# Optimization experiments

Hardware: AMD Instinct MI355X
Metric: run time of the kernel (lower is better)

The kernel has to match this reference:

```python
import jax, jax.numpy as jnp
import numpy as np

N_NODES = 100000
N_EDGES = 625000
D = 128       # in_features == edim
OUT = 2       # out_classes

def setup_inputs() -> dict:
    key = jax.random.key(0)
    k1, k2, k3, k4, k5, k6 = jax.random.split(key, 6)
    nfeats = jax.random.normal(k1, (N_NODES, D), dtype=jnp.float32)
    efeats = jax.random.normal(k2, (N_EDGES, D), dtype=jnp.float32)
    src = jax.random.randint(k3, (N_EDGES,), 0, N_NODES, dtype=jnp.int64)
    dst = jax.random.randint(k4, (N_EDGES,), 0, N_NODES, dtype=jnp.int64)
    # nn.Linear(2*D + D, OUT): weight [OUT, 3D], bias [OUT]
    W = jax.random.normal(k5, (OUT, 3 * D), dtype=jnp.float32) * 0.05
    b = jax.random.normal(k6, (OUT,), dtype=jnp.float32) * 0.05
    return {"nfeats": nfeats, "efeats": efeats, "src": src, "dst": dst, "W": W, "b": b}

def reference(nfeats, efeats, src, dst, W, b):
    # gather per-edge endpoint features, concat with edge feats (residual=True)
    h_src = nfeats[src]            # [E, D]
    h_dst = nfeats[dst]            # [E, D]
    h = jnp.concatenate([h_src, h_dst, efeats], axis=-1)  # [E, 3D]
    score = h @ W.T + b            # [E, OUT]
    return score
```

## Files before the change

kernel.cpp:

```cpp
#include <hip/hip_runtime.h>


static constexpr int D = 128;
static constexpr int THREADS = 256;
static constexpr int GPB = THREADS / 32;

typedef float f32x4 __attribute__((ext_vector_type(4)));

__global__ __launch_bounds__(THREADS) void node_partial_kernel(
    const float* __restrict__ nfeats,
    const float* __restrict__ W,
    float*       __restrict__ pf,
    int N)
{
    const int sl   = threadIdx.x & 31;
    const int gib  = threadIdx.x >> 5;
    const int g0   = blockIdx.x * GPB + gib;
    const int ngrp = gridDim.x * GPB;

    const float4 w0s = *reinterpret_cast<const float4*>(W +   0 + 4 * sl);
    const float4 w1s = *reinterpret_cast<const float4*>(W + 384 + 4 * sl);
    const float4 w0d = *reinterpret_cast<const float4*>(W + 128 + 4 * sl);
    const float4 w1d = *reinterpret_cast<const float4*>(W + 384 + 128 + 4 * sl);

    for (int n = g0 * 2; n + 1 < N; n += ngrp * 2) {
        float v[8];
        #pragma unroll
        for (int j = 0; j < 2; ++j) {
            const f32x4 h = __builtin_nontemporal_load(
                reinterpret_cast<const f32x4*>(nfeats + (size_t)(n + j) * D + 4 * sl));
            v[j*4+0] = h.x * w0s.x + h.y * w0s.y + h.z * w0s.z + h.w * w0s.w;
            v[j*4+1] = h.x * w1s.x + h.y * w1s.y + h.z * w1s.z + h.w * w1s.w;
            v[j*4+2] = h.x * w0d.x + h.y * w0d.y + h.z * w0d.z + h.w * w0d.w;
            v[j*4+3] = h.x * w1d.x + h.y * w1d.y + h.z * w1d.z + h.w * w1d.w;
        }
        float a4[4];
        #pragma unroll
        for (int c = 0; c < 4; ++c) {
            float send = (sl & 16) ? v[c] : v[c+4];
            float keep = (sl & 16) ? v[c+4] : v[c];
            a4[c] = keep + __shfl_xor(send, 16);
        }
        float a2[2];
        #pragma unroll
        for (int c = 0; c < 2; ++c) {
            float send = (sl & 8) ? a4[c] : a4[c+2];
            float keep = (sl & 8) ? a4[c+2] : a4[c];
            a2[c] = keep + __shfl_xor(send, 8);
        }
        float y;
        {
            float send = (sl & 4) ? a2[0] : a2[1];
            float keep = (sl & 4) ? a2[1] : a2[0];
            y = keep + __shfl_xor(send, 4);
        }
        y += __shfl_xor(y, 2);
        y += __shfl_xor(y, 1);
        if ((sl & 3) == 0) {
            pf[4 * (size_t)n + (sl >> 2)] = y;
        }
    }
}

__global__ __launch_bounds__(THREADS) void edge_kernel(
    const float*  __restrict__ efeats,
    const int*    __restrict__ src,
    const int*    __restrict__ dst,
    const float*  __restrict__ W,
    const float*  __restrict__ bias,
    const float*  __restrict__ pf,
    float*        __restrict__ out,
    int E)
{
    const int sl   = threadIdx.x & 31;
    const int gib  = threadIdx.x >> 5;
    const int g0   = blockIdx.x * GPB + gib;
    const int ngrp = gridDim.x * GPB;
    const int step = ngrp * 8;

    const float4 w0e = *reinterpret_cast<const float4*>(W + 256 + 4 * sl);
    const float4 w1e = *reinterpret_cast<const float4*>(W + 384 + 256 + 4 * sl);

    const bool wr   = (sl & 1) == 0;
    const int  myj  = sl >> 2;
    const int  myo  = (sl >> 1) & 1;
    const float myb = myo ? bias[1] : bias[0];

    int e = g0 * 8;
    if (e + 7 >= E) return;

    f32x4 he[8];
    #pragma unroll
    for (int j = 0; j < 8; ++j)
        he[j] = __builtin_nontemporal_load(
            reinterpret_cast<const f32x4*>(efeats + (size_t)(e + j) * D + 4 * sl));
    int sidx = 0, didx = 0;
    if (wr) {
        sidx = src[e + myj];
        didx = dst[e + myj];
    }

    while (e + 7 < E) {
        const int  en   = e + step;
        const bool more = (en + 7 < E);

        float ps = 0.f, pd = 0.f;
        if (wr) {
            ps = pf[(size_t)sidx * 4 + myo];
            pd = pf[(size_t)didx * 4 + 2 + myo];
        }

        float v[16];
        #pragma unroll
        for (int j = 0; j < 8; ++j) {
            v[2*j]   = he[j].x * w0e.x + he[j].y * w0e.y + he[j].z * w0e.z + he[j].w * w0e.w;
            v[2*j+1] = he[j].x * w1e.x + he[j].y * w1e.y + he[j].z * w1e.z + he[j].w * w1e.w;
        }

        if (more) {
            #pragma unroll
            for (int j = 0; j < 8; ++j)
                he[j] = __builtin_nontemporal_load(
                    reinterpret_cast<const f32x4*>(efeats + (size_t)(en + j) * D + 4 * sl));
            if (wr) {
                sidx = src[en + myj];
                didx = dst[en + myj];
            }
        }

        float a8[8];
        #pragma unroll
        for (int c = 0; c < 8; ++c) {
            float send = (sl & 16) ? v[c] : v[c+8];
            float keep = (sl & 16) ? v[c+8] : v[c];
            a8[c] = keep + __shfl_xor(send, 16);
        }
        float a4[4];
        #pragma unroll
        for (int c = 0; c < 4; ++c) {
            float send = (sl & 8) ? a8[c] : a8[c+4];
            float keep = (sl & 8) ? a8[c+4] : a8[c];
            a4[c] = keep + __shfl_xor(send, 8);
        }
        float a2[2];
        #pragma unroll
        for (int c = 0; c < 2; ++c) {
            float send = (sl & 4) ? a4[c] : a4[c+2];
            float keep = (sl & 4) ? a4[c+2] : a4[c];
            a2[c] = keep + __shfl_xor(send, 4);
        }
        float y;
        {
            float send = (sl & 2) ? a2[0] : a2[1];
            float keep = (sl & 2) ? a2[1] : a2[0];
            y = keep + __shfl_xor(send, 2);
        }
        y += __shfl_xor(y, 1);

        if (wr) {
            out[2 * (size_t)e + (sl >> 1)] = y + ps + pd + myb;
        }

        e = en;
    }
}

__global__ __launch_bounds__(THREADS) void mlp_pred_fused_kernel(
    const float* __restrict__ nfeats, const float* __restrict__ efeats,
    const int* __restrict__ src, const int* __restrict__ dst,
    const float* __restrict__ W, const float* __restrict__ bias,
    float* __restrict__ out, int E)
{
    const int sl = threadIdx.x & 31;
    const int gib = threadIdx.x >> 5;
    const int g0 = blockIdx.x * GPB + gib;
    const int ngrp = gridDim.x * GPB;

    const float4 w0s = *reinterpret_cast<const float4*>(W +   0 + 4 * sl);
    const float4 w0d = *reinterpret_cast<const float4*>(W + 128 + 4 * sl);
    const float4 w0e = *reinterpret_cast<const float4*>(W + 256 + 4 * sl);
    const float4 w1s = *reinterpret_cast<const float4*>(W + 384 +   0 + 4 * sl);
    const float4 w1d = *reinterpret_cast<const float4*>(W + 384 + 128 + 4 * sl);
    const float4 w1e = *reinterpret_cast<const float4*>(W + 384 + 256 + 4 * sl);
    const float b0 = bias[0];
    const float b1 = bias[1];

    for (int e = g0; e < E; e += ngrp) {
        const int si = src[e];
        const int di = dst[e];
        const float4 hs = *reinterpret_cast<const float4*>(nfeats + (size_t)si * D + 4 * sl);
        const float4 hd = *reinterpret_cast<const float4*>(nfeats + (size_t)di * D + 4 * sl);
        const float4 he = *reinterpret_cast<const float4*>(efeats + (size_t)e  * D + 4 * sl);

        float a0 = hs.x * w0s.x + hs.y * w0s.y + hs.z * w0s.z + hs.w * w0s.w;
        a0 += hd.x * w0d.x + hd.y * w0d.y + hd.z * w0d.z + hd.w * w0d.w;
        a0 += he.x * w0e.x + he.y * w0e.y + he.z * w0e.z + he.w * w0e.w;
        float a1 = hs.x * w1s.x + hs.y * w1s.y + hs.z * w1s.z + hs.w * w1s.w;
        a1 += hd.x * w1d.x + hd.y * w1d.y + hd.z * w1d.z + hd.w * w1d.w;
        a1 += he.x * w1e.x + he.y * w1e.y + he.z * w1e.z + he.w * w1e.w;

        #pragma unroll
        for (int off = 16; off; off >>= 1) {
            a0 += __shfl_xor(a0, off);
            a1 += __shfl_xor(a1, off);
        }
        if (sl == 0)
            *reinterpret_cast<float2*>(out + 2 * (size_t)e) = make_float2(a0 + b0, a1 + b1);
    }
}

extern "C" void kernel_launch(void* const* d_in, const int* in_sizes, int n_in,
                              void* d_out, int out_size, void* d_ws, size_t ws_size,
                              hipStream_t stream) {
    const float* nfeats = (const float*)d_in[0];
    const float* efeats = (const float*)d_in[1];
    const int*   src    = (const int*)d_in[2];
    const int*   dst    = (const int*)d_in[3];
    const float* W      = (const float*)d_in[4];
    const float* bias   = (const float*)d_in[5];
    float*       out    = (float*)d_out;

    const int E = in_sizes[2];
    const int N = in_sizes[0] / D;

    const size_t p_bytes = (size_t)N * 4 * sizeof(float);

    if (ws_size >= p_bytes && (E & 7) == 0 && (N & 1) == 0) {
        float* pf = (float*)d_ws;

        int groups1 = N / 2;
        int blocks1 = (groups1 + GPB - 1) / GPB;
        if (blocks1 > 2048) blocks1 = 2048;
        node_partial_kernel<<<blocks1, THREADS, 0, stream>>>(nfeats, W, pf, N);

        int groups2 = E / 8;
        int blocks2 = (groups2 + GPB - 1) / GPB;
        if (blocks2 > 2048) blocks2 = 2048;
        edge_kernel<<<blocks2, THREADS, 0, stream>>>(efeats, src, dst, W, bias, pf, out, E);
    } else {
        int blocks = (E + GPB - 1) / GPB;
        if (blocks > 2048) blocks = 2048;
        mlp_pred_fused_kernel<<<blocks, THREADS, 0, stream>>>(nfeats, efeats, src, dst, W, bias, out, E);
    }
}
```

Baseline: 71.74 us.

## Double-buffer edge feature loads and prefetch node rows in partial kernel

The edge kernel now keeps two register batches of edge features and indices, issuing loads two iterations ahead so more memory requests are in flight per wave. The node partial kernel gains a one-iteration software prefetch of its node rows, and output stores become nontemporal. The goal is to hide HBM latency in this bandwidth-bound streaming workload. The cost is higher register pressure from holding two 8x float4 batches, which may reduce occupancy.

After: 70.66 us. Within noise of the previous version (-1.5%).

```diff
diff --git a/kernel.cpp b/kernel.cpp
--- a/kernel.cpp
+++ b/kernel.cpp
@@ -6,6 +6,60 @@
 static constexpr int GPB = THREADS / 32;
 
 typedef float f32x4 __attribute__((ext_vector_type(4)));
+
+__device__ __forceinline__ void load_batch(f32x4 (&he)[8], const float* __restrict__ efeats,
+                                           int e, int sl) {
+    #pragma unroll
+    for (int j = 0; j < 8; ++j)
+        he[j] = __builtin_nontemporal_load(
+            reinterpret_cast<const f32x4*>(efeats + (size_t)(e + j) * D + 4 * sl));
+}
+
+__device__ __forceinline__ void fma_batch(float (&v)[16], const f32x4 (&he)[8],
+                                          const float4& w0e, const float4& w1e) {
+    #pragma unroll
+    for (int j = 0; j < 8; ++j) {
+        v[2*j]   = he[j].x * w0e.x + he[j].y * w0e.y + he[j].z * w0e.z + he[j].w * w0e.w;
+        v[2*j+1] = he[j].x * w1e.x + he[j].y * w1e.y + he[j].z * w1e.z + he[j].w * w1e.w;
+    }
+}
+
+__device__ __forceinline__ void fold_store(const float (&v)[16], int sl, bool wr,
+                                           float ps, float pd, float myb,
+                                           float* __restrict__ out, int e) {
+    float a8[8];
+    #pragma unroll
+    for (int c = 0; c < 8; ++c) {
+        float send = (sl & 16) ? v[c] : v[c+8];
+        float keep = (sl & 16) ? v[c+8] : v[c];
+        a8[c] = keep + __shfl_xor(send, 16);
+    }
+    float a4[4];
+    #pragma unroll
+    for (int c = 0; c < 4; ++c) {
+        float send = (sl & 8) ? a8[c] : a8[c+4];
+        float keep = (sl & 8) ? a8[c+4] : a8[c];
+        a4[c] = keep + __shfl_xor(send, 8);
+    }
+    float a2[2];
+    #pragma unroll
+    for (int c = 0; c < 2; ++c) {
+        float send = (sl & 4) ? a4[c] : a4[c+2];
+        float keep = (sl & 4) ? a4[c+2] : a4[c];
+        a2[c] = keep + __shfl_xor(send, 4);
+    }
+    float y;
+    {
+        float send = (sl & 2) ? a2[0] : a2[1];
+        float keep = (sl & 2) ? a2[1] : a2[0];
+        y = keep + __shfl_xor(send, 2);
+    }
+    y += __shfl_xor(y, 1);
+
+    if (wr) {
+        __builtin_nontemporal_store(y + ps + pd + myb, out + 2 * (size_t)e + (sl >> 1));
+    }
+}
 
 __global__ __launch_bounds__(THREADS) void node_partial_kernel(
     const float* __restrict__ nfeats,
@@ -17,23 +71,40 @@
     const int gib  = threadIdx.x >> 5;
     const int g0   = blockIdx.x * GPB + gib;
     const int ngrp = gridDim.x * GPB;
+    const int nstep = ngrp * 2;
 
     const float4 w0s = *reinterpret_cast<const float4*>(W +   0 + 4 * sl);
     const float4 w1s = *reinterpret_cast<const float4*>(W + 384 + 4 * sl);
     const float4 w0d = *reinterpret_cast<const float4*>(W + 128 + 4 * sl);
     const float4 w1d = *reinterpret_cast<const float4*>(W + 384 + 128 + 4 * sl);
 
-    for (int n = g0 * 2; n + 1 < N; n += ngrp * 2) {
+    int n = g0 * 2;
+    if (n + 1 >= N) return;
+
+    f32x4 h[2];
+    #pragma unroll
+    for (int j = 0; j < 2; ++j)
+        h[j] = __builtin_nontemporal_load(
+            reinterpret_cast<const f32x4*>(nfeats + (size_t)(n + j) * D + 4 * sl));
+
+    while (n + 1 < N) {
         float v[8];
         #pragma unroll
         for (int j = 0; j < 2; ++j) {
-            const f32x4 h = __builtin_nontemporal_load(
-                reinterpret_cast<const f32x4*>(nfeats + (size_t)(n + j) * D + 4 * sl));
-            v[j*4+0] = h.x * w0s.x + h.y * w0s.y + h.z * w0s.z + h.w * w0s.w;
-            v[j*4+1] = h.x * w1s.x + h.y * w1s.y + h.z * w1s.z + h.w * w1s.w;
-            v[j*4+2] = h.x * w0d.x + h.y * w0d.y + h.z * w0d.z + h.w * w0d.w;
-            v[j*4+3] = h.x * w1d.x + h.y * w1d.y + h.z * w1d.z + h.w * w1d.w;
-        }
+            v[j*4+0] = h[j].x * w0s.x + h[j].y * w0s.y + h[j].z * w0s.z + h[j].w * w0s.w;
+            v[j*4+1] = h[j].x * w1s.x + h[j].y * w1s.y + h[j].z * w1s.z + h[j].w * w1s.w;
+            v[j*4+2] = h[j].x * w0d.x + h[j].y * w0d.y + h[j].z * w0d.z + h[j].w * w0d.w;
+            v[j*4+3] = h[j].x * w1d.x + h[j].y * w1d.y + h[j].z * w1d.z + h[j].w * w1d.w;
+        }
+
+        const int nn = n + nstep;
+        if (nn + 1 < N) {
+            #pragma unroll
+            for (int j = 0; j < 2; ++j)
+                h[j] = __builtin_nontemporal_load(
+                    reinterpret_cast<const f32x4*>(nfeats + (size_t)(nn + j) * D + 4 * sl));
+        }
+
         float a4[4];
         #pragma unroll
         for (int c = 0; c < 4; ++c) {
@@ -59,6 +130,7 @@
         if ((sl & 3) == 0) {
             pf[4 * (size_t)n + (sl >> 2)] = y;
         }
+        n = nn;
     }
 }
 
@@ -89,79 +161,52 @@
     int e = g0 * 8;
     if (e + 7 >= E) return;
 
-    f32x4 he[8];
-    #pragma unroll
-    for (int j = 0; j < 8; ++j)
-        he[j] = __builtin_nontemporal_load(
-            reinterpret_cast<const f32x4*>(efeats + (size_t)(e + j) * D + 4 * sl));
-    int sidx = 0, didx = 0;
-    if (wr) {
-        sidx = src[e + myj];
-        didx = dst[e + myj];
-    }
-
-    while (e + 7 < E) {
-        const int  en   = e + step;
-        const bool more = (en + 7 < E);
-
-        float ps = 0.f, pd = 0.f;
-        if (wr) {
-            ps = pf[(size_t)sidx * 4 + myo];
-            pd = pf[(size_t)didx * 4 + 2 + myo];
-        }
-
-        float v[16];
-        #pragma unroll
-        for (int j = 0; j < 8; ++j) {
-            v[2*j]   = he[j].x * w0e.x + he[j].y * w0e.y + he[j].z * w0e.z + he[j].w * w0e.w;
-            v[2*j+1] = he[j].x * w1e.x + he[j].y * w1e.y + he[j].z * w1e.z + he[j].w * w1e.w;
-        }
-
-        if (more) {
-            #pragma unroll
-            for (int j = 0; j < 8; ++j)
-                he[j] = __builtin_nontemporal_load(
-                    reinterpret_cast<const f32x4*>(efeats + (size_t)(en + j) * D + 4 * sl));
+    f32x4 heA[8], heB[8];
+    int sA = 0, dA = 0, sB = 0, dB = 0;
+
+    load_batch(heA, efeats, e, sl);
+    if (wr) { sA = src[e + myj]; dA = dst[e + myj]; }
+    if (e + step + 7 < E) {
+        load_batch(heB, efeats, e + step, sl);
+        if (wr) { sB = src[e + step + myj]; dB = dst[e + step + myj]; }
+    }
+
+    for (;;) {
+        {
+            float ps = 0.f, pd = 0.f;
             if (wr) {
-                sidx = src[en + myj];
-                didx = dst[en + myj];
-            }
-        }
-
-        float a8[8];
-        #pragma unroll
-        for (int c = 0; c < 8; ++c) {
-            float send = (sl & 16) ? v[c] : v[c+8];
-            float keep = (sl & 16) ? v[c+8] : v[c];
-            a8[c] = keep + __shfl_xor(send, 16);
-        }
-        float a4[4];
-        #pragma unroll
-        for (int c = 0; c < 4; ++c) {
-            float send = (sl & 8) ? a8[c] : a8[c+4];
-            float keep = (sl & 8) ? a8[c+4] : a8[c];
-            a4[c] = keep + __shfl_xor(send, 8);
-        }
-        float a2[2];
-        #pragma unroll
-        for (int c = 0; c < 2; ++c) {
-            float send = (sl & 4) ? a4[c] : a4[c+2];
-            float keep = (sl & 4) ? a4[c+2] : a4[c];
-            a2[c] = keep + __shfl_xor(send, 4);
-        }
-        float y;
+                ps = pf[(size_t)sA * 4 + myo];
+                pd = pf[(size_t)dA * 4 + 2 + myo];
+            }
+            float v[16];
+            fma_batch(v, heA, w0e, w1e);
+            const int ep = e + 2 * step;
+            if (ep + 7 < E) {
+                load_batch(heA, efeats, ep, sl);
+                if (wr) { sA = src[ep + myj]; dA = dst[ep + myj]; }
+            }
+            fold_store(v, sl, wr, ps, pd, myb, out, e);
+        }
+        e += step;
+        if (e + 7 >= E) break;
+
         {
-            float send = (sl & 2) ? a2[0] : a2[1];
-            float keep = (sl & 2) ? a2[1] : a2[0];
-            y = keep + __shfl_xor(send, 2);
-        }
-        y += __shfl_xor(y, 1);
-
-        if (wr) {
-            out[2 * (size_t)e + (sl >> 1)] = y + ps + pd + myb;
-        }
-
-        e = en;
+            float ps = 0.f, pd = 0.f;
+            if (wr) {
+                ps = pf[(size_t)sB * 4 + myo];
+                pd = pf[(size_t)dB * 4 + 2 + myo];
+            }
+            float v[16];
+            fma_batch(v, heB, w0e, w1e);
+            const int ep = e + 2 * step;
+            if (ep + 7 < E) {
+                load_batch(heB, efeats, ep, sl);
+                if (wr) { sB = src[ep + myj]; dB = dst[ep + myj]; }
+            }
+            fold_store(v, sl, wr, ps, pd, myb, out, e);
+        }
+        e += step;
+        if (e + 7 >= E) break;
     }
 }
 
```
